# Kernel optimization log

Hardware: AMD Instinct MI355X
Metric: run time of the kernel (lower is better)

The kernel has to match this reference:

```python
import jax, jax.numpy as jnp
import numpy as np

N, S, D = 8, 448, 768
VS, DS = 50000, 256
VP, DP = 200, 128
VM, DM = 400, 128
VA, DA = 360, 128
EPS_LS = 0.1
LN_EPS = 1e-12
SQRT2 = 1.4142135623730951


def setup_inputs() -> dict:
    key = jax.random.key(0)
    ks = jax.random.split(key, 20)
    total = N * S
    # all sequence lengths == S; next-token prediction uses tokens [0, S-2] as
    # inputs (hidden_sel) and tokens [1, S-1] as targets (target_sel)
    hidden_sel = np.concatenate([i * S + np.arange(S - 1) for i in range(N)]).astype(np.int32)
    target_sel = np.concatenate([i * S + np.arange(1, S) for i in range(N)]).astype(np.int32)
    tokens_lengths = (np.arange(total) % 4).astype(np.int32)  # per-token affix counts
    affix_sel = np.nonzero(tokens_lengths[target_sel] > 0)[0].astype(np.int32)

    def p(k, shape):
        return jax.random.normal(k, shape, jnp.float32) * 0.02

    inp = {
        "tr_hidden_state": jax.random.normal(ks[0], (S, N, D), jnp.float32),
        "affixes_prob": jax.random.uniform(ks[1], (total, VA), dtype=jnp.float32),
        "stems": jax.random.randint(ks[2], (total,), 0, VS, jnp.int32),
        "pos_tags": jax.random.randint(ks[3], (total,), 0, VP, jnp.int32),
        "lm_morphs": jax.random.randint(ks[4], (total,), 0, VM, jnp.int32),
        "hidden_sel_idx": jnp.asarray(hidden_sel),
        "target_sel_idx": jnp.asarray(target_sel),
        "affix_sel_idx": jnp.asarray(affix_sel),
        # stem head
        "stem_emb": p(ks[5], (VS, DS)), "stem_W": p(ks[6], (D, DS)),
        "stem_b": jnp.zeros((DS,)), "stem_g": jnp.ones((DS,)),
        "stem_beta": jnp.zeros((DS,)), "stem_bias": jnp.zeros((VS,)),
        # pos-tag head
        "pos_emb": p(ks[7], (VP, DP)), "pos_W": p(ks[8], (D, DP)),
        "pos_b": jnp.zeros((DP,)), "pos_g": jnp.ones((DP,)),
        "pos_beta": jnp.zeros((DP,)), "pos_bias": jnp.zeros((VP,)),
        # lm-morph head
        "morph_emb": p(ks[9], (VM, DM)), "morph_W": p(ks[10], (D, DM)),
        "morph_b": jnp.zeros((DM,)), "morph_g": jnp.ones((DM,)),
        "morph_beta": jnp.zeros((DM,)), "morph_bias": jnp.zeros((VM,)),
        # affixes head
        "aff_emb": p(ks[11], (VA, DA)), "aff_W": p(ks[12], (D, DA)),
        "aff_b": jnp.zeros((DA,)), "aff_g": jnp.ones((DA,)),
        "aff_beta": jnp.zeros((DA,)), "aff_bias": jnp.zeros((VA,)),
    }
    return inp


def _gelu(x):
    return x * 0.5 * (1.0 + jax.lax.erf(x / SQRT2))


def _ln(x, g, b):
    m = x.mean(-1, keepdims=True)
    v = ((x - m) ** 2).mean(-1, keepdims=True)
    return (x - m) * jax.lax.rsqrt(v + LN_EPS) * g + b


def _head(x, W, b, g, beta, emb, bias):
    h = _ln(_gelu(x @ W + b), g, beta)  # BaseHeadTransform
    return h @ emb.T + bias             # tied decoder + bias


def _ls_nll(lprobs, tgt):
    # label_smoothed_nll_loss with reduce=True, no ignore_index
    nll = -jnp.take_along_axis(lprobs, tgt[:, None], axis=1)[:, 0]
    smooth = -lprobs.sum(-1)
    nll_m, sm_m = nll.mean(), smooth.mean()
    eps_i = EPS_LS / (lprobs.shape[-1] - 1)
    return (1.0 - EPS_LS - eps_i) * nll_m + eps_i * sm_m, nll_m


def reference(tr_hidden_state, affixes_prob, stems, pos_tags, lm_morphs,
              hidden_sel_idx, target_sel_idx, affix_sel_idx,
              stem_emb, stem_W, stem_b, stem_g, stem_beta, stem_bias,
              pos_emb, pos_W, pos_b, pos_g, pos_beta, pos_bias,
              morph_emb, morph_W, morph_b, morph_g, morph_beta, morph_bias,
              aff_emb, aff_W, aff_b, aff_g, aff_beta, aff_bias):
    flat = jnp.transpose(tr_hidden_state, (1, 0, 2)).reshape(N * S, D)
    x = flat[hidden_sel_idx]  # [T, D] ragged gather of predictor states

    stem_lp = jax.nn.log_softmax(_head(x, stem_W, stem_b, stem_g, stem_beta, stem_emb, stem_bias), axis=-1)
    stem_loss, stem_nll = _ls_nll(stem_lp, stems[target_sel_idx])

    pos_lp = jax.nn.log_softmax(_head(x, pos_W, pos_b, pos_g, pos_beta, pos_emb, pos_bias), axis=-1)
    pos_loss, pos_nll = _ls_nll(pos_lp, pos_tags[target_sel_idx])

    morph_lp = jax.nn.log_softmax(_head(x, morph_W, morph_b, morph_g, morph_beta, morph_emb, morph_bias), axis=-1)
    morph_loss, morph_nll = _ls_nll(morph_lp, lm_morphs[target_sel_idx])

    xa = x[affix_sel_idx]                                # tokens with affixes
    ta = affixes_prob[target_sel_idx][affix_sel_idx]     # [Ta, VA]
    z = _head(xa, aff_W, aff_b, aff_g, aff_beta, aff_emb, aff_bias)
    aff_loss = jnp.mean(jnp.maximum(z, 0.0) - z * ta + jnp.log1p(jnp.exp(-jnp.abs(z))))

    return jnp.stack([stem_loss, pos_loss, morph_loss, aff_loss, stem_nll, pos_nll, morph_nll])
```

## Files before the change

kernel.cpp:

```cpp
#include <hip/hip_runtime.h>
#include <cstdint>
#include <cstddef>


typedef __attribute__((ext_vector_type(8))) __bf16 bf16x8;
typedef __attribute__((ext_vector_type(4))) float f32x4;
typedef __attribute__((ext_vector_type(4))) unsigned short u16x4;
typedef __attribute__((ext_vector_type(2))) unsigned short u16x2;

namespace {
constexpr int S_LEN   = 448;
constexpr int N_SEQ   = 8;
constexpr int D_MODEL = 768;
constexpr int TPAD    = 3584;
constexpr int VS = 50000, VP = 200, VM = 400, VA = 360;
constexpr int DS_STEM = 256, DS_POS = 128, DS_MORPH = 128, DS_AFF = 128;
constexpr int VS_PAD = 50176;
constexpr int VCHUNK = 32;
constexpr int VITERS = 3136 / VCHUNK;
constexpr float PAD_E = (float)(VS_PAD - VS);
constexpr int NVB_P = 1;
constexpr int NVB_M = 2;
constexpr float LOG2E = 1.4426950408889634f;
constexpr float LN2   = 0.6931471805599453f;
constexpr int B_STEM = 448;
constexpr int B_P    = B_STEM + 112;
constexpr int B_M    = B_P + 224;
constexpr int PREP_G = TPAD * D_MODEL / 256;
constexpr int PREP_T = PREP_G + 491520 / 256;
constexpr int PREP_C = PREP_T + 12753;
}

__device__ __forceinline__ unsigned short f2bf(float f) {
  unsigned int u = __float_as_uint(f);
  unsigned int r = (u + 0x7FFFu + ((u >> 16) & 1u)) >> 16;
  return (unsigned short)r;
}
__device__ __forceinline__ float bf2f(unsigned short u) {
  return __uint_as_float(((unsigned int)u) << 16);
}

__global__ __launch_bounds__(256) void prep_kernel(
    const float* __restrict__ tr, const int* __restrict__ hsel,
    const int* __restrict__ tsel, const int* __restrict__ asel,
    const int* __restrict__ stems, const int* __restrict__ postags,
    const int* __restrict__ morphs,
    unsigned short* __restrict__ x, int* __restrict__ tgtS, int* __restrict__ tgtP,
    int* __restrict__ tgtM, int* __restrict__ arow, int T, int Ta,
    const float* __restrict__ sW, const float* __restrict__ pW,
    const float* __restrict__ mW, const float* __restrict__ aW,
    unsigned short* __restrict__ wtS, unsigned short* __restrict__ wtP,
    unsigned short* __restrict__ wtM, unsigned short* __restrict__ wtA,
    const float* __restrict__ sE, const float* __restrict__ pE,
    const float* __restrict__ mE, const float* __restrict__ aE,
    const float* __restrict__ sb,
    unsigned short* __restrict__ dS, unsigned short* __restrict__ dP,
    unsigned short* __restrict__ dM, unsigned short* __restrict__ dA,
    float* __restrict__ bp) {
  const int bid = blockIdx.x;
  if (bid < PREP_G) {
    const size_t e = (size_t)bid * 256 + threadIdx.x;
    const int t = (int)(e / D_MODEL);
    const int d = (int)(e % D_MODEL);
    float v = 0.f;
    if (t < T) {
      int idx = hsel[t];
      int n = idx / S_LEN, s = idx % S_LEN;
      v = tr[((size_t)s * N_SEQ + n) * D_MODEL + d];
    }
    x[e] = f2bf(v);
    if (e < (size_t)T) {
      int tt = tsel[e];
      tgtS[e] = stems[tt]; tgtP[e] = postags[tt]; tgtM[e] = morphs[tt];
    }
    if (e < (size_t)Ta) arow[e] = tsel[asel[e]];
  } else if (bid < PREP_T) {
    const int e = (bid - PREP_G) * 256 + threadIdx.x;
    const float* W; unsigned short* Wt; int DS; int local;
    if (e < 196608)      { W = sW; Wt = wtS; DS = 256; local = e; }
    else if (e < 294912) { W = pW; Wt = wtP; DS = 128; local = e - 196608; }
    else if (e < 393216) { W = mW; Wt = wtM; DS = 128; local = e - 294912; }
    else                 { W = aW; Wt = wtA; DS = 128; local = e - 393216; }
    const int n = local / D_MODEL, k = local % D_MODEL;
    Wt[local] = f2bf(W[(size_t)k * DS + n]);
  } else {
    const size_t q = ((size_t)(bid - PREP_T) * 256 + threadIdx.x) * 4;
    if (q >= 13008896) {
      const size_t local = q - 13008896;
      float4 v = make_float4(0.f, 0.f, 0.f, 0.f);
      if (local < (size_t)VS) v = *(const float4*)(sb + local);
      v.x *= LOG2E; v.y *= LOG2E; v.z *= LOG2E; v.w *= LOG2E;
      *(float4*)(bp + local) = v;
      return;
    }
    const float* src; unsigned short* dst; size_t local, real;
    float sc = 1.f;
    if (q < 12845056)      { src = sE; dst = dS; local = q;            real = 12800000; sc = LOG2E; }
    else if (q < 12877824) { src = pE; dst = dP; local = q - 12845056; real = 25600; }
    else if (q < 12943360) { src = mE; dst = dM; local = q - 12877824; real = 51200; }
    else                   { src = aE; dst = dA; local = q - 12943360; real = 46080; }
    float4 v = make_float4(0.f, 0.f, 0.f, 0.f);
    if (local < real) v = *(const float4*)(src + local);
    u16x4 o = { f2bf(v.x * sc), f2bf(v.y * sc), f2bf(v.z * sc), f2bf(v.w * sc) };
    *(u16x4*)(dst + local) = o;
  }
}

template <int NT>
__device__ __forceinline__ void head_body(
    const unsigned short* __restrict__ x, const unsigned short* __restrict__ Wt,
    const float* __restrict__ bvec, const float* __restrict__ gvec,
    const float* __restrict__ betav, unsigned short* __restrict__ hout) {
  constexpr int DS = NT * 16;
  const int lane = threadIdx.x & 63;
  const int wave = threadIdx.x >> 6;
  const int row0 = blockIdx.x * 32 + wave * 16;
  const int lrow = lane & 15;
  const int lk8  = (lane >> 4) * 8;

  f32x4 acc[NT];
#pragma unroll
  for (int nt = 0; nt < NT; ++nt) acc[nt] = f32x4{0.f, 0.f, 0.f, 0.f};

  const unsigned short* xrow = x + (size_t)(row0 + lrow) * D_MODEL + lk8;
#pragma unroll
  for (int ks = 0; ks < 24; ++ks) {
    bf16x8 a = *(const bf16x8*)(xrow + ks * 32);
#pragma unroll
    for (int nt = 0; nt < NT; ++nt) {
      bf16x8 b = *(const bf16x8*)(Wt + (size_t)(nt * 16 + lrow) * D_MODEL + ks * 32 + lk8);
      acc[nt] = __builtin_amdgcn_mfma_f32_16x16x32_bf16(a, b, acc[nt], 0, 0, 0);
    }
  }

  float bb[NT], gg[NT], be[NT];
#pragma unroll
  for (int nt = 0; nt < NT; ++nt) {
    int c = nt * 16 + lrow;
    bb[nt] = bvec[c]; gg[nt] = gvec[c]; be[nt] = betav[c];
  }
#pragma unroll
  for (int r = 0; r < 4; ++r) {
    const int row = row0 + (lane >> 4) * 4 + r;
    float vals[NT];
    float s = 0.f, s2 = 0.f;
#pragma unroll
    for (int nt = 0; nt < NT; ++nt) {
      float v = acc[nt][r] + bb[nt];
      v = 0.5f * v * (1.f + erff(v * 0.70710678118654752f));
      vals[nt] = v; s += v; s2 += v * v;
    }
    s  += __shfl_xor(s, 1);  s  += __shfl_xor(s, 2);  s  += __shfl_xor(s, 4);  s  += __shfl_xor(s, 8);
    s2 += __shfl_xor(s2, 1); s2 += __shfl_xor(s2, 2); s2 += __shfl_xor(s2, 4); s2 += __shfl_xor(s2, 8);
    const float mean = s * (1.f / DS);
    const float var  = s2 * (1.f / DS) - mean * mean;
    const float rstd = rsqrtf(var + 1e-12f);
#pragma unroll
    for (int nt = 0; nt < NT; ++nt) {
      float o = (vals[nt] - mean) * rstd * gg[nt] + be[nt];
      hout[(size_t)row * DS + nt * 16 + lrow] = f2bf(o);
    }
  }
}

__global__ __launch_bounds__(128, 2) void head_all_kernel(
    const unsigned short* __restrict__ x,
    const unsigned short* __restrict__ wtS, const float* __restrict__ sb,
    const float* __restrict__ sg, const float* __restrict__ sbe, unsigned short* __restrict__ hS,
    const unsigned short* __restrict__ wtP, const float* __restrict__ pb,
    const float* __restrict__ pg, const float* __restrict__ pbe, unsigned short* __restrict__ hP,
    const unsigned short* __restrict__ wtM, const float* __restrict__ mb,
    const float* __restrict__ mg, const float* __restrict__ mbe, unsigned short* __restrict__ hM,
    const unsigned short* __restrict__ wtA, const float* __restrict__ ab,
    const float* __restrict__ ag, const float* __restrict__ abe, unsigned short* __restrict__ hA) {
  if (blockIdx.y == 3)      head_body<16>(x, wtS, sb, sg, sbe, hS);
  else if (blockIdx.y == 0) head_body<8>(x, wtP, pb, pg, pbe, hP);
  else if (blockIdx.y == 1) head_body<8>(x, wtM, mb, mg, mbe, hM);
  else                      head_body<8>(x, wtA, ab, ag, abe, hA);
}


__device__ __forceinline__ void stem_role(
    const unsigned short* __restrict__ h, const unsigned short* __restrict__ emb,
    const float* __restrict__ bpad, float* __restrict__ psum,
    float* __restrict__ psum2, char* smem) {
  unsigned short (*lbuf)[4096] = (unsigned short(*)[4096])smem;
  float* lbias = (float*)(smem + 32768);

  const int f    = blockIdx.x;
  const int xcd  = f & 7;
  const int m    = f >> 3;
  const int bx   = m % 14;
  const int by   = (m / 14) * 8 + xcd;
  const int tid  = threadIdx.x;
  const int lane = tid & 63;
  const int wave = tid >> 6;
  const int lrow = lane & 15;
  const int hi   = lane >> 4;
  const int lk8  = hi * 8;
  const int tok0 = bx * 256 + wave * 64;
  const int vbase0 = by * (VITERS * 16);

  for (int i = tid; i < VITERS * 16; i += 256) lbias[i] = bpad[vbase0 + i];

  bf16x8 hB[4][8];
#pragma unroll
  for (int tt = 0; tt < 4; ++tt)
#pragma unroll
    for (int ks = 0; ks < 8; ++ks)
      hB[tt][ks] = *(const bf16x8*)(h + (size_t)(tok0 + tt * 16 + lrow) * 256 + ks * 32 + lk8);

  const int d0 = tid * 16;
  const int s0 = d0 ^ (((d0 >> 9) & 7) << 4);
  const char* gsA = (const char*)emb + (size_t)vbase0 * 512 + s0;
  const char* gsB = gsA + 4096;

  auto stage = [&](int buf, int it) {
    __builtin_amdgcn_global_load_lds(
        (const __attribute__((address_space(1))) unsigned int*)(gsA + (size_t)it * 8192),
        (__attribute__((address_space(3))) unsigned int*)(smem + buf * 8192 + wave * 1024),
        16, 0, 0);
    __builtin_amdgcn_global_load_lds(
        (const __attribute__((address_space(1))) unsigned int*)(gsB + (size_t)it * 8192),
        (__attribute__((address_space(3))) unsigned int*)(smem + buf * 8192 + 4096 + wave * 1024),
        16, 0, 0);
  };

  int loff[8];
#pragma unroll
  for (int ks = 0; ks < 8; ++ks)
    loff[ks] = (lrow * 512 + ks * 64 + hi * 16) ^ ((lrow & 7) << 4);

  float esum[4] = {0.f, 0.f, 0.f, 0.f};
  float ssum[4] = {0.f, 0.f, 0.f, 0.f};

  stage(0, 0); stage(1, 1); stage(2, 2);
  __syncthreads();

#pragma unroll 1
  for (int it = 0; it < VITERS; ++it) {
    if (it < VITERS - 2)       asm volatile("s_waitcnt vmcnt(4)" ::: "memory");
    else if (it == VITERS - 2) asm volatile("s_waitcnt vmcnt(2)" ::: "memory");
    else                       asm volatile("s_waitcnt vmcnt(0)" ::: "memory");
    __builtin_amdgcn_s_barrier();

    const float4 bv = *(const float4*)(lbias + it * 16 + hi * 4);
    const char* lp = (const char*)&lbuf[it & 3][0];
    bf16x8 aA[8];
#pragma unroll
    for (int ks = 0; ks < 8; ++ks)
      aA[ks] = *(const bf16x8*)(lp + loff[ks]);

    if (it + 3 < VITERS) stage((it + 3) & 3, it + 3);

#pragma unroll
    for (int tt = 0; tt < 4; ++tt) {
      f32x4 acc = f32x4{bv.x, bv.y, bv.z, bv.w};
#pragma unroll
      for (int ks = 0; ks < 8; ++ks)
        acc = __builtin_amdgcn_mfma_f32_16x16x32_bf16(aA[ks], hB[tt][ks], acc, 0, 0, 0);
      esum[tt] += (exp2f(acc[0]) + exp2f(acc[1])) + (exp2f(acc[2]) + exp2f(acc[3]));
      ssum[tt] += (acc[0] + acc[1]) + (acc[2] + acc[3]);
    }
  }

#pragma unroll
  for (int tt = 0; tt < 4; ++tt) {
    float e = esum[tt], s = ssum[tt];
    e += __shfl_xor(e, 16); e += __shfl_xor(e, 32);
    s += __shfl_xor(s, 16); s += __shfl_xor(s, 32);
    if (hi == 0) {
      const int tok = tok0 + tt * 16 + lrow;
      psum [(size_t)tok * VCHUNK + by] = e;
      psum2[(size_t)tok * VCHUNK + by] = s * LN2;
    }
  }
}

__device__ __forceinline__ void pm_role(
    const unsigned short* __restrict__ h, const unsigned short* __restrict__ emb,
    const float* __restrict__ bias, float* __restrict__ psum,
    float* __restrict__ psum2, int V, int NVB, int vbx, int vby, char* smem) {
  const int tid = threadIdx.x;
  const int lane = tid & 63;
  const int wave4 = tid >> 6;
  const int colbase = vby * 256 + wave4 * 64;
  const int row0 = vbx * 32;
  const int lrow = lane & 15;
  const int hi   = lane >> 4;
  const int lk8  = hi * 8;
  float (*lds_e)[32] = (float(*)[32])smem;
  float (*lds_s)[32] = (float(*)[32])(smem + 512);

  bf16x8 bfr[4][4];
  float bv[4];
  bool mk[4];
#pragma unroll
  for (int nt = 0; nt < 4; ++nt) {
    int col = colbase + nt * 16 + lrow;
#pragma unroll
    for (int ks = 0; ks < 4; ++ks)
      bfr[ks][nt] = *(const bf16x8*)(emb + (size_t)col * 128 + ks * 32 + lk8);
    mk[nt] = (col < V);
    bv[nt] = mk[nt] ? bias[col] : 0.f;
  }

  f32x4 acc[2][4];
#pragma unroll
  for (int rt = 0; rt < 2; ++rt)
#pragma unroll
    for (int nt = 0; nt < 4; ++nt) acc[rt][nt] = f32x4{0.f, 0.f, 0.f, 0.f};

  const unsigned short* hrow = h + (size_t)(row0 + lrow) * 128 + lk8;
#pragma unroll
  for (int ks = 0; ks < 4; ++ks) {
#pragma unroll
    for (int rt = 0; rt < 2; ++rt) {
      bf16x8 a = *(const bf16x8*)(hrow + (size_t)rt * 16 * 128 + ks * 32);
#pragma unroll
      for (int nt = 0; nt < 4; ++nt)
        acc[rt][nt] = __builtin_amdgcn_mfma_f32_16x16x32_bf16(a, bfr[ks][nt], acc[rt][nt], 0, 0, 0);
    }
  }

#pragma unroll
  for (int rt = 0; rt < 2; ++rt)
#pragma unroll
    for (int r = 0; r < 4; ++r) {
      float e = 0.f, s = 0.f;
#pragma unroll
      for (int nt = 0; nt < 4; ++nt) {
        float v = acc[rt][nt][r] + bv[nt];
        float ev = __expf(v);
        e += mk[nt] ? ev : 0.f;
        s += mk[nt] ? v : 0.f;
      }
      e += __shfl_xor(e, 1); e += __shfl_xor(e, 2); e += __shfl_xor(e, 4); e += __shfl_xor(e, 8);
      s += __shfl_xor(s, 1); s += __shfl_xor(s, 2); s += __shfl_xor(s, 4); s += __shfl_xor(s, 8);
      if (lrow == 0) {
        lds_e[wave4][rt * 16 + hi * 4 + r] = e;
        lds_s[wave4][rt * 16 + hi * 4 + r] = s;
      }
    }
  __syncthreads();
  if (tid < 32) {
    const int rr = tid;
    float e = lds_e[0][rr] + lds_e[1][rr] + lds_e[2][rr] + lds_e[3][rr];
    float s = lds_s[0][rr] + lds_s[1][rr] + lds_s[2][rr] + lds_s[3][rr];
    const int row = row0 + rr;
    psum [(size_t)row * NVB + vby] = e;
    psum2[(size_t)row * NVB + vby] = s;
  }
}

__device__ __forceinline__ void aff_role(
    const unsigned short* __restrict__ h, const unsigned short* __restrict__ emb,
    const float* __restrict__ bias, const int* __restrict__ asel,
    const int* __restrict__ arow, const float* __restrict__ aprob,
    float* __restrict__ partial, int Ta, int gaff, int bx, int grp, char* smem) {
  const int tid = threadIdx.x;
  const int lane = tid & 63;
  const int wave4 = tid >> 6;
  const int colbase = grp * 256 + wave4 * 64;
  const int lrow = lane & 15;
  const int lk8  = (lane >> 4) * 8;
  float* wred = (float*)smem;

  bf16x8 bfr[4][4];
  float bv[4];
  bool mk[4];
#pragma unroll
  for (int nt = 0; nt < 4; ++nt) {
    int col = colbase + nt * 16 + lrow;
#pragma unroll
    for (int ks = 0; ks < 4; ++ks)
      bfr[ks][nt] = *(const bf16x8*)(emb + (size_t)col * DS_AFF + ks * 32 + lk8);
    mk[nt] = (col < VA);
    bv[nt] = mk[nt] ? bias[col] : 0.f;
  }

  float lsum = 0.f;
  {
    const int rb = bx * 16;
    const int ia = rb + lrow;
    const int srow = (ia < Ta) ? asel[ia] : 0;
    f32x4 acc[4];
#pragma unroll
    for (int nt = 0; nt < 4; ++nt) acc[nt] = f32x4{0.f, 0.f, 0.f, 0.f};
    const unsigned short* hrow = h + (size_t)srow * DS_AFF + lk8;
#pragma unroll
    for (int ks = 0; ks < 4; ++ks) {
      bf16x8 a = *(const bf16x8*)(hrow + ks * 32);
#pragma unroll
      for (int nt = 0; nt < 4; ++nt)
        acc[nt] = __builtin_amdgcn_mfma_f32_16x16x32_bf16(a, bfr[ks][nt], acc[nt], 0, 0, 0);
    }
#pragma unroll
    for (int r = 0; r < 4; ++r) {
      const int i2 = rb + (lane >> 4) * 4 + r;
      const bool live = (i2 < Ta);
      const int trow = live ? arow[i2] : 0;
#pragma unroll
      for (int nt = 0; nt < 4; ++nt) {
        if (live && mk[nt]) {
          float z = acc[nt][r] + bv[nt];
          float ta = aprob[(size_t)trow * VA + (colbase + nt * 16 + lrow)];
          lsum += fmaxf(z, 0.f) - z * ta + log1pf(__expf(-fabsf(z)));
        }
      }
    }
  }
#pragma unroll
  for (int m = 1; m < 64; m <<= 1) lsum += __shfl_xor(lsum, m);
  if (lane == 0) wred[wave4] = lsum;
  __syncthreads();
  if (tid == 0)
    partial[grp * gaff + bx] = wred[0] + wred[1] + wred[2] + wred[3];
}

__device__ __forceinline__ void tgt_role(
    const unsigned short* __restrict__ hS, const unsigned short* __restrict__ embS,
    const float* __restrict__ bS, const int* __restrict__ tgtS_,
    const unsigned short* __restrict__ hP, const unsigned short* __restrict__ embP,
    const float* __restrict__ bP, const int* __restrict__ tgtP_,
    const unsigned short* __restrict__ hM, const unsigned short* __restrict__ embM,
    const float* __restrict__ bM, const int* __restrict__ tgtM_,
    float* __restrict__ tlog, int T, int vb) {
  const int lane = threadIdx.x & 63;
  const int wave = threadIdx.x >> 6;
  const int t = vb * 4 + wave;
  if (t >= T) return;
  const int tg = tgtS_[t], tp = tgtP_[t], tm = tgtM_[t];
  u16x4 hv = *(const u16x4*)(hS + (size_t)t * 256 + lane * 4);
  u16x4 ev = *(const u16x4*)(embS + (size_t)tg * 256 + lane * 4);
  float d0 = bf2f(hv[0]) * bf2f(ev[0]) + bf2f(hv[1]) * bf2f(ev[1]) +
             bf2f(hv[2]) * bf2f(ev[2]) + bf2f(hv[3]) * bf2f(ev[3]);
  u16x2 hp = *(const u16x2*)(hP + (size_t)t * 128 + lane * 2);
  u16x2 ep = *(const u16x2*)(embP + (size_t)tp * 128 + lane * 2);
  float d1 = bf2f(hp[0]) * bf2f(ep[0]) + bf2f(hp[1]) * bf2f(ep[1]);
  u16x2 hm = *(const u16x2*)(hM + (size_t)t * 128 + lane * 2);
  u16x2 em = *(const u16x2*)(embM + (size_t)tm * 128 + lane * 2);
  float d2 = bf2f(hm[0]) * bf2f(em[0]) + bf2f(hm[1]) * bf2f(em[1]);
#pragma unroll
  for (int m = 1; m < 64; m <<= 1) {
    d0 += __shfl_xor(d0, m); d1 += __shfl_xor(d1, m); d2 += __shfl_xor(d2, m);
  }
  if (lane == 0) {
    tlog[t]            = d0 * LN2 + bS[tg];
    tlog[TPAD + t]     = d1 + bP[tp];
    tlog[2 * TPAD + t] = d2 + bM[tm];
  }
}

__global__ __launch_bounds__(256, 2) void mega_stats_kernel(
    const unsigned short* __restrict__ hS, const unsigned short* __restrict__ embS,
    const float* __restrict__ bpadS, float* __restrict__ psS, float* __restrict__ ps2S,
    const unsigned short* __restrict__ hP, const unsigned short* __restrict__ embP,
    const float* __restrict__ p_bias, float* __restrict__ psP, float* __restrict__ ps2P,
    const unsigned short* __restrict__ hM, const unsigned short* __restrict__ embM,
    const float* __restrict__ m_bias, float* __restrict__ psM, float* __restrict__ ps2M,
    const unsigned short* __restrict__ hA, const unsigned short* __restrict__ embA,
    const float* __restrict__ a_bias, const int* __restrict__ asel,
    const int* __restrict__ arow, const float* __restrict__ aprob,
    float* __restrict__ affp,
    const float* __restrict__ s_bias, const int* __restrict__ tgtS,
    const int* __restrict__ tgtP, const int* __restrict__ tgtM,
    float* __restrict__ tlog, int T, int Ta, int gaff) {
  __shared__ alignas(16) char smem_[39040];
  const int bid = blockIdx.x;
  if (bid < B_STEM) {
    stem_role(hS, embS, bpadS, psS, ps2S, smem_);
  } else if (bid < B_P) {
    pm_role(hP, embP, p_bias, psP, ps2P, VP, NVB_P, bid - B_STEM, 0, smem_);
  } else if (bid < B_M) {
    const int b = bid - B_P;
    pm_role(hM, embM, m_bias, psM, ps2M, VM, NVB_M, b >> 1, b & 1, smem_);
  } else if (bid < B_M + 2 * gaff) {
    const int b = bid - B_M;
    aff_role(hA, embA, a_bias, asel, arow, aprob, affp, Ta, gaff, b >> 1, b & 1, smem_);
  } else {
    tgt_role(hS, embS, s_bias, tgtS, hP, embP, p_bias, tgtP,
             hM, embM, m_bias, tgtM, tlog, T, bid - B_M - 2 * gaff);
  }
}

__global__ __launch_bounds__(256) void combine2_kernel(
    const float* __restrict__ psS, const float* __restrict__ ps2S,
    const float* __restrict__ psP, const float* __restrict__ ps2P,
    const float* __restrict__ psM, const float* __restrict__ ps2M,
    const float* __restrict__ tlog,
    float* __restrict__ nll, float* __restrict__ sm, int T) {
  const int lane = threadIdx.x & 63;
  const int wave = threadIdx.x >> 6;
  const int t = blockIdx.x * 4 + wave;
  if (t >= T) return;

  float z = 0.f, s = 0.f;
  if (lane < VCHUNK) {
    z = psS[(size_t)t * VCHUNK + lane];
    s = ps2S[(size_t)t * VCHUNK + lane];
  }
#pragma unroll
  for (int m = 1; m < 64; m <<= 1) { z += __shfl_xor(z, m); s += __shfl_xor(s, m); }
  if (lane == 0) {
    z -= PAD_E;
    float lz = logf(z);
    nll[t] = lz - tlog[t];
    sm[t]  = (float)VS * lz - s;

    float zP = psP[t], sP = ps2P[t];
    float lzP = logf(zP);
    nll[TPAD + t] = lzP - tlog[TPAD + t];
    sm[TPAD + t]  = (float)VP * lzP - sP;

    float zM = psM[2 * t] + psM[2 * t + 1];
    float sM = ps2M[2 * t] + ps2M[2 * t + 1];
    float lzM = logf(zM);
    nll[2 * TPAD + t] = lzM - tlog[2 * TPAD + t];
    sm[2 * TPAD + t]  = (float)VM * lzM - sM;
  }
}

__global__ __launch_bounds__(256) void finalize_kernel(
    const float* __restrict__ nll, const float* __restrict__ sm,
    const float* __restrict__ affp, int naff, float* __restrict__ out, int T, int Ta) {
  __shared__ float red[256];
  const int tid = threadIdx.x;
  float nll_m[3], sm_m[3];
  for (int h2 = 0; h2 < 3; ++h2) {
    float a = 0.f, b = 0.f;
    for (int t = tid; t < T; t += 256) { a += nll[h2 * TPAD + t]; b += sm[h2 * TPAD + t]; }
    red[tid] = a; __syncthreads();
    for (int s = 128; s > 0; s >>= 1) { if (tid < s) red[tid] += red[tid + s]; __syncthreads(); }
    float asum = red[0]; __syncthreads();
    red[tid] = b; __syncthreads();
    for (int s = 128; s > 0; s >>= 1) { if (tid < s) red[tid] += red[tid + s]; __syncthreads(); }
    float bsm = red[0]; __syncthreads();
    nll_m[h2] = asum / (float)T;
    sm_m[h2]  = bsm / (float)T;
  }
  float av = 0.f;
  for (int i = tid; i < naff; i += 256) av += affp[i];
  red[tid] = av; __syncthreads();
  for (int s = 128; s > 0; s >>= 1) { if (tid < s) red[tid] += red[tid + s]; __syncthreads(); }
  if (tid == 0) {
    const float Vv[3] = {(float)VS, (float)VP, (float)VM};
    for (int h2 = 0; h2 < 3; ++h2) {
      float eps_i = 0.1f / (Vv[h2] - 1.f);
      out[h2] = (1.0f - 0.1f - eps_i) * nll_m[h2] + eps_i * sm_m[h2];
      out[4 + h2] = nll_m[h2];
    }
    out[3] = red[0] / ((float)Ta * (float)VA);
  }
}

extern "C" void kernel_launch(void* const* d_in, const int* in_sizes, int n_in,
                              void* d_out, int out_size, void* d_ws, size_t ws_size,
                              hipStream_t stream) {
  const float* tr      = (const float*)d_in[0];
  const float* aprob   = (const float*)d_in[1];
  const int* stems     = (const int*)d_in[2];
  const int* postags   = (const int*)d_in[3];
  const int* morphs    = (const int*)d_in[4];
  const int* hsel      = (const int*)d_in[5];
  const int* tsel      = (const int*)d_in[6];
  const int* asel      = (const int*)d_in[7];
  const float* s_emb = (const float*)d_in[8],  *s_W = (const float*)d_in[9];
  const float* s_b   = (const float*)d_in[10], *s_g = (const float*)d_in[11];
  const float* s_be  = (const float*)d_in[12], *s_bias = (const float*)d_in[13];
  const float* p_emb = (const float*)d_in[14], *p_W = (const float*)d_in[15];
  const float* p_b   = (const float*)d_in[16], *p_g = (const float*)d_in[17];
  const float* p_be  = (const float*)d_in[18], *p_bias = (const float*)d_in[19];
  const float* m_emb = (const float*)d_in[20], *m_W = (const float*)d_in[21];
  const float* m_b   = (const float*)d_in[22], *m_g = (const float*)d_in[23];
  const float* m_be  = (const float*)d_in[24], *m_bias = (const float*)d_in[25];
  const float* a_emb = (const float*)d_in[26], *a_W = (const float*)d_in[27];
  const float* a_b   = (const float*)d_in[28], *a_g = (const float*)d_in[29];
  const float* a_be  = (const float*)d_in[30], *a_bias = (const float*)d_in[31];

  const int T  = in_sizes[5];
  const int Ta = in_sizes[7];

  size_t off = 0;
  auto alloc = [&](size_t nbytes) -> char* {
    char* p = (char*)d_ws + off;
    off = (off + nbytes + 255) & ~(size_t)255;
    return p;
  };
  unsigned short* x    = (unsigned short*)alloc((size_t)TPAD * D_MODEL * 2);
  unsigned short* wtS  = (unsigned short*)alloc((size_t)DS_STEM * D_MODEL * 2);
  unsigned short* wtP  = (unsigned short*)alloc((size_t)DS_POS * D_MODEL * 2);
  unsigned short* wtM  = (unsigned short*)alloc((size_t)DS_MORPH * D_MODEL * 2);
  unsigned short* wtA  = (unsigned short*)alloc((size_t)DS_AFF * D_MODEL * 2);
  unsigned short* embS = (unsigned short*)alloc((size_t)VS_PAD * DS_STEM * 2);
  unsigned short* embP = (unsigned short*)alloc((size_t)256 * DS_POS * 2);
  unsigned short* embM = (unsigned short*)alloc((size_t)512 * DS_MORPH * 2);
  unsigned short* embA = (unsigned short*)alloc((size_t)512 * DS_AFF * 2);
  unsigned short* hS   = (unsigned short*)alloc((size_t)TPAD * DS_STEM * 2);
  unsigned short* hP   = (unsigned short*)alloc((size_t)TPAD * DS_POS * 2);
  unsigned short* hM   = (unsigned short*)alloc((size_t)TPAD * DS_MORPH * 2);
  unsigned short* hA   = (unsigned short*)alloc((size_t)TPAD * DS_AFF * 2);
  float* bpadS = (float*)alloc((size_t)VS_PAD * 4);
  float* psS   = (float*)alloc((size_t)TPAD * VCHUNK * 4);
  float* ps2S  = (float*)alloc((size_t)TPAD * VCHUNK * 4);
  float* psP   = (float*)alloc((size_t)TPAD * NVB_P * 4);
  float* ps2P  = (float*)alloc((size_t)TPAD * NVB_P * 4);
  float* psM   = (float*)alloc((size_t)TPAD * NVB_M * 4);
  float* ps2M  = (float*)alloc((size_t)TPAD * NVB_M * 4);
  float* tlog  = (float*)alloc((size_t)3 * TPAD * 4);
  int*   tgtS  = (int*)alloc((size_t)TPAD * 4);
  int*   tgtP  = (int*)alloc((size_t)TPAD * 4);
  int*   tgtM  = (int*)alloc((size_t)TPAD * 4);
  int*   arow  = (int*)alloc((size_t)TPAD * 4);
  float* nllb  = (float*)alloc((size_t)3 * TPAD * 4);
  float* smb   = (float*)alloc((size_t)3 * TPAD * 4);
  float* affp  = (float*)alloc(2048);
  (void)ws_size; (void)n_in; (void)out_size;

  const int gaff = (Ta + 15) / 16;
  const int tgtb = (T + 3) / 4;

  prep_kernel<<<PREP_C, 256, 0, stream>>>(
      tr, hsel, tsel, asel, stems, postags, morphs, x, tgtS, tgtP, tgtM, arow, T, Ta,
      s_W, p_W, m_W, a_W, wtS, wtP, wtM, wtA,
      s_emb, p_emb, m_emb, a_emb, s_bias, embS, embP, embM, embA, bpadS);
  head_all_kernel<<<dim3(TPAD / 32, 4), 128, 0, stream>>>(
      x, wtS, s_b, s_g, s_be, hS, wtP, p_b, p_g, p_be, hP,
      wtM, m_b, m_g, m_be, hM, wtA, a_b, a_g, a_be, hA);
  mega_stats_kernel<<<B_M + 2 * gaff + tgtb, 256, 0, stream>>>(
      hS, embS, bpadS, psS, ps2S,
      hP, embP, p_bias, psP, ps2P,
      hM, embM, m_bias, psM, ps2M,
      hA, embA, a_bias, asel, arow, aprob, affp,
      s_bias, tgtS, tgtP, tgtM, tlog, T, Ta, gaff);
  combine2_kernel<<<(T + 3) / 4, 256, 0, stream>>>(psS, ps2S, psP, ps2P, psM, ps2M, tlog, nllb, smb, T);
  finalize_kernel<<<1, 256, 0, stream>>>(nllb, smb, affp, gaff * 2, (float*)d_out, T, Ta);
}
```

Baseline: 244.2 us.

## Process two stem vocab tiles per barrier with a six-buffer LDS ring

The stem head's streaming loop now handles two 16-row embedding tiles per iteration, using a six-slot LDS ring arranged as three pairs and prefetching two pairs ahead. This halves the number of waitcnt and barrier synchronisations. It also replaces exp2f with the raw hardware exp2 builtin to avoid range-handling overhead. The cost is more LDS per block (about 55 KB) and more registers for the second A fragment, which could limit occupancy under the two-blocks-per-CU launch bound.

Result: faster. 226.1 us (-7.4%).

```diff
diff --git a/kernel.cpp b/kernel.cpp
--- a/kernel.cpp
+++ b/kernel.cpp
@@ -18,6 +18,7 @@
 constexpr int VS_PAD = 50176;
 constexpr int VCHUNK = 32;
 constexpr int VITERS = 3136 / VCHUNK;
+constexpr int PERIODS = VITERS / 2;
 constexpr float PAD_E = (float)(VS_PAD - VS);
 constexpr int NVB_P = 1;
 constexpr int NVB_M = 2;
@@ -38,6 +39,13 @@
 }
 __device__ __forceinline__ float bf2f(unsigned short u) {
   return __uint_as_float(((unsigned int)u) << 16);
+}
+__device__ __forceinline__ float fexp2(float x) {
+#if __has_builtin(__builtin_amdgcn_exp2f)
+  return __builtin_amdgcn_exp2f(x);
+#else
+  return exp2f(x);
+#endif
 }
 
 __global__ __launch_bounds__(256) void prep_kernel(
@@ -184,8 +192,7 @@
     const unsigned short* __restrict__ h, const unsigned short* __restrict__ emb,
     const float* __restrict__ bpad, float* __restrict__ psum,
     float* __restrict__ psum2, char* smem) {
-  unsigned short (*lbuf)[4096] = (unsigned short(*)[4096])smem;
-  float* lbias = (float*)(smem + 32768);
+  float* lbias = (float*)(smem + 49152);
 
   const int f    = blockIdx.x;
   const int xcd  = f & 7;
@@ -215,13 +222,13 @@
   const char* gsA = (const char*)emb + (size_t)vbase0 * 512 + s0;
   const char* gsB = gsA + 4096;
 
-  auto stage = [&](int buf, int it) {
+  auto stage_tile = [&](int buf, int tile) {
     __builtin_amdgcn_global_load_lds(
-        (const __attribute__((address_space(1))) unsigned int*)(gsA + (size_t)it * 8192),
+        (const __attribute__((address_space(1))) unsigned int*)(gsA + (size_t)tile * 8192),
         (__attribute__((address_space(3))) unsigned int*)(smem + buf * 8192 + wave * 1024),
         16, 0, 0);
     __builtin_amdgcn_global_load_lds(
-        (const __attribute__((address_space(1))) unsigned int*)(gsB + (size_t)it * 8192),
+        (const __attribute__((address_space(1))) unsigned int*)(gsB + (size_t)tile * 8192),
         (__attribute__((address_space(3))) unsigned int*)(smem + buf * 8192 + 4096 + wave * 1024),
         16, 0, 0);
   };
@@ -234,32 +241,56 @@
   float esum[4] = {0.f, 0.f, 0.f, 0.f};
   float ssum[4] = {0.f, 0.f, 0.f, 0.f};
 
-  stage(0, 0); stage(1, 1); stage(2, 2);
+  stage_tile(0, 0); stage_tile(1, 1);
+  stage_tile(2, 2); stage_tile(3, 3);
   __syncthreads();
 
 #pragma unroll 1
-  for (int it = 0; it < VITERS; ++it) {
-    if (it < VITERS - 2)       asm volatile("s_waitcnt vmcnt(4)" ::: "memory");
-    else if (it == VITERS - 2) asm volatile("s_waitcnt vmcnt(2)" ::: "memory");
-    else                       asm volatile("s_waitcnt vmcnt(0)" ::: "memory");
+  for (int p = 0; p < PERIODS; ++p) {
+    if (p < PERIODS - 1) asm volatile("s_waitcnt vmcnt(4)" ::: "memory");
+    else                 asm volatile("s_waitcnt vmcnt(0)" ::: "memory");
     __builtin_amdgcn_s_barrier();
 
-    const float4 bv = *(const float4*)(lbias + it * 16 + hi * 4);
-    const char* lp = (const char*)&lbuf[it & 3][0];
+    const int t0 = 2 * p, t1 = 2 * p + 1;
+    const int b0 = (p % 3) * 2, b1 = b0 + 1;
+    const float4 bv0 = *(const float4*)(lbias + t0 * 16 + hi * 4);
+    const float4 bv1 = *(const float4*)(lbias + t1 * 16 + hi * 4);
+
+    const char* lp0 = smem + b0 * 8192;
     bf16x8 aA[8];
 #pragma unroll
     for (int ks = 0; ks < 8; ++ks)
-      aA[ks] = *(const bf16x8*)(lp + loff[ks]);
-
-    if (it + 3 < VITERS) stage((it + 3) & 3, it + 3);
+      aA[ks] = *(const bf16x8*)(lp0 + loff[ks]);
 
 #pragma unroll
     for (int tt = 0; tt < 4; ++tt) {
-      f32x4 acc = f32x4{bv.x, bv.y, bv.z, bv.w};
+      f32x4 acc = f32x4{bv0.x, bv0.y, bv0.z, bv0.w};
 #pragma unroll
       for (int ks = 0; ks < 8; ++ks)
         acc = __builtin_amdgcn_mfma_f32_16x16x32_bf16(aA[ks], hB[tt][ks], acc, 0, 0, 0);
-      esum[tt] += (exp2f(acc[0]) + exp2f(acc[1])) + (exp2f(acc[2]) + exp2f(acc[3]));
+      esum[tt] += (fexp2(acc[0]) + fexp2(acc[1])) + (fexp2(acc[2]) + fexp2(acc[3]));
+      ssum[tt] += (acc[0] + acc[1]) + (acc[2] + acc[3]);
+    }
+
+    const char* lp1 = smem + b1 * 8192;
+    bf16x8 aB[8];
+#pragma unroll
+    for (int ks = 0; ks < 8; ++ks)
+      aB[ks] = *(const bf16x8*)(lp1 + loff[ks]);
+
+    if (p + 2 < PERIODS) {
+      const int nb = ((p + 2) % 3) * 2;
+      stage_tile(nb,     2 * (p + 2));
+      stage_tile(nb + 1, 2 * (p + 2) + 1);
+    }
+
+#pragma unroll
+    for (int tt = 0; tt < 4; ++tt) {
+      f32x4 acc = f32x4{bv1.x, bv1.y, bv1.z, bv1.w};
+#pragma unroll
+      for (int ks = 0; ks < 8; ++ks)
+        acc = __builtin_amdgcn_mfma_f32_16x16x32_bf16(aB[ks], hB[tt][ks], acc, 0, 0, 0);
+      esum[tt] += (fexp2(acc[0]) + fexp2(acc[1])) + (fexp2(acc[2]) + fexp2(acc[3]));
       ssum[tt] += (acc[0] + acc[1]) + (acc[2] + acc[3]);
     }
   }
@@ -466,7 +497,7 @@
     const float* __restrict__ s_bias, const int* __restrict__ tgtS,
     const int* __restrict__ tgtP, const int* __restrict__ tgtM,
     float* __restrict__ tlog, int T, int Ta, int gaff) {
-  __shared__ alignas(16) char smem_[39040];
+  __shared__ alignas(16) char smem_[55424];
   const int bid = blockIdx.x;
   if (bid < B_STEM) {
     stem_role(hS, embS, bpadS, psS, ps2S, smem_);
```
